# Kernel tuning notes

Measured on AMD Instinct MI355X. Metric: run time of the kernel, lower is better.

The kernel has to match this reference:

```python
import jax, jax.numpy as jnp
import numpy as np

N_HEAD = 16
HEAD_DIM = 64
D_MODEL = N_HEAD * HEAD_DIM  # 1024
B, L = 2, 2048

def setup_inputs() -> dict:
    key = jax.random.key(0)
    k1, k2, k3, k4, k5 = jax.random.split(key, 5)
    s = 0.02
    return {
        "hidden_states": jax.random.normal(k1, (B, L, D_MODEL), dtype=jnp.float32),
        "W_qkv": jax.random.normal(k2, (D_MODEL, 3 * D_MODEL), dtype=jnp.float32) * s,
        "b_qkv": jax.random.normal(k3, (3 * D_MODEL,), dtype=jnp.float32) * s,
        "W_proj": jax.random.normal(k4, (D_MODEL, D_MODEL), dtype=jnp.float32) * s,
        "b_proj": jax.random.normal(k5, (D_MODEL,), dtype=jnp.float32) * s,
        "window_size": 128,
    }

def reference(hidden_states, W_qkv, b_qkv, W_proj, b_proj, window_size):
    Bb, Ll, Dd = hidden_states.shape
    # GPT-2 Conv1D: x @ W + b
    qkv = hidden_states @ W_qkv + b_qkv  # [B, L, 3D]
    q, k, v = jnp.split(qkv, 3, axis=2)
    def to_heads(t):
        return t.reshape(Bb, Ll, N_HEAD, HEAD_DIM).transpose(0, 2, 1, 3)  # [B,H,L,d]
    q, k, v = to_heads(q), to_heads(k), to_heads(v)
    scale = jnp.sqrt(jnp.asarray(HEAD_DIM, dtype=q.dtype))
    scores = jnp.einsum('bhqd,bhkd->bhqk', q, k) / scale  # [B,H,L,L]
    pos = jnp.arange(Ll)
    dist = pos[:, None] - pos[None, :]  # query - key
    sw_mask = (dist < 0) | (dist >= window_size)  # True = masked out
    scores = jnp.where(sw_mask[None, None, :, :], jnp.asarray(-jnp.inf, scores.dtype), scores)
    attn_weights = jax.nn.softmax(scores, axis=-1)  # dropout is identity (eval)
    out = jnp.einsum('bhqk,bhkd->bhqd', attn_weights, v)  # [B,H,L,d]
    out = out.transpose(0, 2, 1, 3).reshape(Bb, Ll, Dd)
    out = out @ W_proj + b_proj
    return (out, attn_weights)
```

## Files before the change

### kernel.cpp

```cpp
#include <hip/hip_runtime.h>
#include <stdint.h>

#define NH 16
#define HD 64
#define DM 1024
#define BB 2
#define LL 2048

typedef __bf16 bf16x8 __attribute__((ext_vector_type(8)));
typedef float f32x4 __attribute__((ext_vector_type(4)));

__device__ __forceinline__ uint16_t f2bf(float f) {
  union { float f; uint32_t u; } x{f};
  uint32_t r = (x.u + 0x7fff + ((x.u >> 16) & 1)) >> 16;
  return (uint16_t)r;
}

__device__ __forceinline__ void gload_lds16(const void* g, void* l) {
  __builtin_amdgcn_global_load_lds(
      (const __attribute__((address_space(1))) unsigned int*)g,
      (__attribute__((address_space(3))) unsigned int*)l, 16, 0, 0);
}

__global__ __launch_bounds__(256) void cvt_bf16(
    const float* __restrict__ x, uint16_t* __restrict__ y, int n4) {
  int i = blockIdx.x * 256 + threadIdx.x;
  if (i >= n4) return;
  float4 v = ((const float4*)x)[i];
  ushort4 o;
  o.x = f2bf(v.x); o.y = f2bf(v.y); o.z = f2bf(v.z); o.w = f2bf(v.w);
  ((ushort4*)y)[i] = o;
}

__global__ __launch_bounds__(256) void transpose_cvt(
    const float* __restrict__ W, uint16_t* __restrict__ WT, int K, int N) {
  __shared__ float t[32][33];
  int bk = blockIdx.y * 32, bn = blockIdx.x * 32;
  int c = threadIdx.x & 31, r0 = threadIdx.x >> 5;
#pragma unroll
  for (int p = 0; p < 4; ++p) {
    int r = r0 + p * 8;
    t[r][c] = W[(size_t)(bk + r) * N + bn + c];
  }
  __syncthreads();
#pragma unroll
  for (int p = 0; p < 4; ++p) {
    int r = r0 + p * 8;
    WT[(size_t)(bn + r) * K + bk + c] = f2bf(t[c][r]);
  }
}

__global__ __launch_bounds__(256) void gemm_bt_bf16(
    const uint16_t* __restrict__ A, const uint16_t* __restrict__ BT,
    const float* __restrict__ bias, float* __restrict__ C,
    int M, int N, int K) {
  __shared__ uint16_t As[128 * 32];
  __shared__ uint16_t Bs[128 * 32];
  const int tid = threadIdx.x;
  const int bm = blockIdx.y * 128, bn = blockIdx.x * 128;
  const int lane = tid & 63, wave = tid >> 6;
  const int wr = wave >> 1, wc = wave & 1;
  f32x4 acc[4][4] = {};

  for (int k0 = 0; k0 < K; k0 += 32) {
#pragma unroll
    for (int c = 0; c < 2; ++c) {
      int e = c * 2048 + tid * 8;
      int r = e >> 5, col = e & 31;
      gload_lds16(A + (size_t)(bm + r) * K + k0 + col, (char*)As + (size_t)e * 2);
      gload_lds16(BT + (size_t)(bn + r) * K + k0 + col, (char*)Bs + (size_t)e * 2);
    }
    __syncthreads();

    const int kseg = (lane >> 4) * 8;
    bf16x8 af[4], bfr[4];
#pragma unroll
    for (int i = 0; i < 4; ++i)
      af[i] = *(const bf16x8*)&As[(wr * 64 + i * 16 + (lane & 15)) * 32 + kseg];
#pragma unroll
    for (int j = 0; j < 4; ++j)
      bfr[j] = *(const bf16x8*)&Bs[(wc * 64 + j * 16 + (lane & 15)) * 32 + kseg];
#pragma unroll
    for (int i = 0; i < 4; ++i)
#pragma unroll
      for (int j = 0; j < 4; ++j)
        acc[i][j] = __builtin_amdgcn_mfma_f32_16x16x32_bf16(af[i], bfr[j], acc[i][j], 0, 0, 0);
    __syncthreads();
  }

#pragma unroll
  for (int i = 0; i < 4; ++i) {
#pragma unroll
    for (int j = 0; j < 4; ++j) {
      int col = bn + wc * 64 + j * 16 + (lane & 15);
      float bv = bias[col];
#pragma unroll
      for (int r = 0; r < 4; ++r) {
        int row = bm + wr * 64 + i * 16 + (lane >> 4) * 4 + r;
        C[(size_t)row * N + col] = acc[i][j][r] + bv;
      }
    }
  }
}

#define QT 32
#define KT 160
#define KS 72
#define PS 168

__global__ __launch_bounds__(256, 4) void attn_sw(
    const float* __restrict__ qkv,
    float* __restrict__ attnw,
    uint16_t* __restrict__ ctxb,
    const int* __restrict__ wsz_p) {
  __shared__ __align__(16) char smemU[KT * KS * 2];
  __shared__ __align__(16) uint16_t Qs[QT * KS];
  __shared__ __align__(16) uint16_t Psb[QT * PS];
  uint16_t* Ksb = (uint16_t*)smemU;
  float* Sf = (float*)smemU;

  const int wsz = *wsz_p;
  const int tid = threadIdx.x;
  const int lane = tid & 63, wave = tid >> 6;
  const int ntile = LL / QT;
  const int qt = blockIdx.x % ntile;
  const int h = (blockIdx.x / ntile) % NH;
  const int b = blockIdx.x / (ntile * NH);
  const int q0 = qt * QT;
  const int kmin = max(0, q0 - (wsz - 1));
  const int kbase = kmin & ~31;

  {
    int r = tid >> 3, c = (tid & 7) * 8;
    const float* src = qkv + (size_t)(b * LL + q0 + r) * (3 * DM) + h * HD + c;
    float4 a = *(const float4*)src, b4 = *(const float4*)(src + 4);
    uint16_t* dst = &Qs[r * KS + c];
    dst[0] = f2bf(a.x); dst[1] = f2bf(a.y); dst[2] = f2bf(a.z); dst[3] = f2bf(a.w);
    dst[4] = f2bf(b4.x); dst[5] = f2bf(b4.y); dst[6] = f2bf(b4.z); dst[7] = f2bf(b4.w);
  }
#pragma unroll
  for (int p = 0; p < 3; ++p) {
    int u = tid + p * 256;
    int r = u >> 2, c = (u & 3) * 16;
    if (r < KT) {
      const float* src = qkv + (size_t)(b * LL + kbase + r) * (3 * DM) + DM + h * HD + c;
      float4 a = *(const float4*)src, b4 = *(const float4*)(src + 4);
      float4 e = *(const float4*)(src + 8), f = *(const float4*)(src + 12);
      uint16_t* dst = &Ksb[r * KS + c];
      dst[0] = f2bf(a.x); dst[1] = f2bf(a.y); dst[2] = f2bf(a.z); dst[3] = f2bf(a.w);
      dst[4] = f2bf(b4.x); dst[5] = f2bf(b4.y); dst[6] = f2bf(b4.z); dst[7] = f2bf(b4.w);
      dst[8] = f2bf(e.x); dst[9] = f2bf(e.y); dst[10] = f2bf(e.z); dst[11] = f2bf(e.w);
      dst[12] = f2bf(f.x); dst[13] = f2bf(f.y); dst[14] = f2bf(f.z); dst[15] = f2bf(f.w);
    }
  }
  __syncthreads();

  const int mt = wave & 1, ntb = (wave >> 1) * 5;
  f32x4 sfrag[5];
  {
    const int kseg = (lane >> 4) * 8;
    bf16x8 aq0 = *(const bf16x8*)&Qs[(mt * 16 + (lane & 15)) * KS + kseg];
    bf16x8 aq1 = *(const bf16x8*)&Qs[(mt * 16 + (lane & 15)) * KS + 32 + kseg];
#pragma unroll
    for (int t = 0; t < 5; ++t) {
      int nt = ntb + t;
      bf16x8 bk0 = *(const bf16x8*)&Ksb[(nt * 16 + (lane & 15)) * KS + kseg];
      bf16x8 bk1 = *(const bf16x8*)&Ksb[(nt * 16 + (lane & 15)) * KS + 32 + kseg];
      f32x4 c = {0.f, 0.f, 0.f, 0.f};
      c = __builtin_amdgcn_mfma_f32_16x16x32_bf16(aq0, bk0, c, 0, 0, 0);
      c = __builtin_amdgcn_mfma_f32_16x16x32_bf16(aq1, bk1, c, 0, 0, 0);
      sfrag[t] = c;
    }
  }
  __syncthreads();

#pragma unroll
  for (int t = 0; t < 5; ++t) {
    int nt = ntb + t;
#pragma unroll
    for (int r = 0; r < 4; ++r)
      Sf[(mt * 16 + (lane >> 4) * 4 + r) * PS + nt * 16 + (lane & 15)] = sfrag[t][r];
  }
  __syncthreads();

  {
    const int qi = tid >> 3;
    const int kg = tid & 7;
    const int q = q0 + qi;
    float s[20];
#pragma unroll
    for (int j = 0; j < 20; ++j) s[j] = Sf[qi * PS + kg + 8 * j];
    float m = -1e30f;
#pragma unroll
    for (int j = 0; j < 20; ++j) {
      int gk = kbase + kg + 8 * j;
      bool valid = (gk <= q) && (gk > q - wsz);
      s[j] = valid ? s[j] * 0.125f : -1e30f;
      m = fmaxf(m, s[j]);
    }
#pragma unroll
    for (int off = 1; off < 8; off <<= 1)
      m = fmaxf(m, __shfl_xor(m, off, 64));
    float l = 0.f;
#pragma unroll
    for (int j = 0; j < 20; ++j) {
      float e = (s[j] > -1e29f) ? __expf(s[j] - m) : 0.f;
      s[j] = e;
      l += e;
    }
#pragma unroll
    for (int off = 1; off < 8; off <<= 1)
      l += __shfl_xor(l, off, 64);
    float inv = 1.f / l;
#pragma unroll
    for (int j = 0; j < 20; ++j) {
      float p = s[j] * inv;
      Sf[qi * PS + kg + 8 * j] = p;
      Psb[qi * PS + kg + 8 * j] = f2bf(p);
    }
  }
  __syncthreads();

  {
#pragma unroll
    for (int it = 0; it < 16; ++it) {
      int r = it * 2 + (tid >> 7);
      size_t rowoff = ((size_t)((b * NH + h) * LL + q0 + r)) * LL;
      int cb = (tid & 127) * 4;
#pragma unroll
      for (int jj = 0; jj < 4; ++jj) {
        int c4 = cb + jj * 512;
        f32x4 v = {0.f, 0.f, 0.f, 0.f};
        int pc = c4 - kbase;
        if (pc >= 0 && pc < KT)
          v = *(const f32x4*)&Sf[r * PS + pc];
        __builtin_nontemporal_store(v, (f32x4*)&attnw[rowoff + c4]);
      }
    }
  }

  {
    const int nt = wave;
    const int kseg = (lane >> 4) * 8;
    f32x4 ofrag[2] = {};
#pragma unroll
    for (int ks = 0; ks < 5; ++ks) {
      const float* vs = qkv + (size_t)(b * LL + kbase + ks * 32 + kseg) * (3 * DM) +
                        2 * DM + h * HD + nt * 16 + (lane & 15);
      uint16_t vb[8];
#pragma unroll
      for (int j = 0; j < 8; ++j) vb[j] = f2bf(vs[(size_t)j * (3 * DM)]);
      bf16x8 bv = *(const bf16x8*)vb;
#pragma unroll
      for (int m = 0; m < 2; ++m) {
        bf16x8 ap = *(const bf16x8*)&Psb[(m * 16 + (lane & 15)) * PS + ks * 32 + kseg];
        ofrag[m] = __builtin_amdgcn_mfma_f32_16x16x32_bf16(ap, bv, ofrag[m], 0, 0, 0);
      }
    }
#pragma unroll
    for (int m = 0; m < 2; ++m)
#pragma unroll
      for (int r = 0; r < 4; ++r) {
        int q = q0 + m * 16 + (lane >> 4) * 4 + r;
        ctxb[(size_t)(b * LL + q) * DM + h * HD + nt * 16 + (lane & 15)] = f2bf(ofrag[m][r]);
      }
  }
}

extern "C" void kernel_launch(void* const* d_in, const int* in_sizes, int n_in,
                              void* d_out, int out_size, void* d_ws, size_t ws_size,
                              hipStream_t stream) {
  const float* hs    = (const float*)d_in[0];
  const float* Wqkv  = (const float*)d_in[1];
  const float* bqkv  = (const float*)d_in[2];
  const float* Wproj = (const float*)d_in[3];
  const float* bproj = (const float*)d_in[4];
  const int*   wszp  = (const int*)d_in[5];

  float* out   = (float*)d_out;
  float* attnw = (float*)d_out + (size_t)BB * LL * DM;

  char* wsb = (char*)d_ws;
  float*    qkv    = (float*)wsb;
  uint16_t* hsctxb = (uint16_t*)(wsb + 50331648);
  uint16_t* WqkvT  = (uint16_t*)(wsb + 50331648 + 8388608);
  uint16_t* WprojT = (uint16_t*)(wsb + 50331648 + 8388608 + 6291456);

  dim3 blk(256);

  cvt_bf16<<<dim3((BB * LL * DM / 4 + 255) / 256), blk, 0, stream>>>(hs, hsctxb, BB * LL * DM / 4);
  transpose_cvt<<<dim3(3 * DM / 32, DM / 32), blk, 0, stream>>>(Wqkv, WqkvT, DM, 3 * DM);
  transpose_cvt<<<dim3(DM / 32, DM / 32), blk, 0, stream>>>(Wproj, WprojT, DM, DM);

  gemm_bt_bf16<<<dim3(3 * DM / 128, BB * LL / 128), blk, 0, stream>>>(
      hsctxb, WqkvT, bqkv, qkv, BB * LL, 3 * DM, DM);

  attn_sw<<<dim3(BB * NH * (LL / QT)), blk, 0, stream>>>(qkv, attnw, hsctxb, wszp);

  gemm_bt_bf16<<<dim3(DM / 128, BB * LL / 128), blk, 0, stream>>>(
      hsctxb, WprojT, bproj, out, BB * LL, DM, DM);
}
```

Baseline: 638.2 us.

## Store QKV as bf16 and split attention-weight expansion into separate kernel

```diff
diff --git a/kernel.cpp b/kernel.cpp
--- a/kernel.cpp
+++ b/kernel.cpp
@@ -14,6 +14,10 @@
   union { float f; uint32_t u; } x{f};
   uint32_t r = (x.u + 0x7fff + ((x.u >> 16) & 1)) >> 16;
   return (uint16_t)r;
+}
+__device__ __forceinline__ float bf2f(uint16_t u) {
+  union { uint32_t u; float f; } x{(uint32_t)u << 16};
+  return x.f;
 }
 
 __device__ __forceinline__ void gload_lds16(const void* g, void* l) {
@@ -52,7 +56,7 @@
 
 __global__ __launch_bounds__(256) void gemm_bt_bf16(
     const uint16_t* __restrict__ A, const uint16_t* __restrict__ BT,
-    const float* __restrict__ bias, float* __restrict__ C,
+    const float* __restrict__ bias, void* __restrict__ Cout, int c_bf16,
     int M, int N, int K) {
   __shared__ uint16_t As[128 * 32];
   __shared__ uint16_t Bs[128 * 32];
@@ -96,8 +100,12 @@
       float bv = bias[col];
 #pragma unroll
       for (int r = 0; r < 4; ++r) {
-        int row = bm + wr * 64 + i * 16 + (lane >> 4) * 4 + r;
-        C[(size_t)row * N + col] = acc[i][j][r] + bv;
+        size_t row = (size_t)(bm + wr * 64 + i * 16 + (lane >> 4) * 4 + r);
+        float v = acc[i][j][r] + bv;
+        if (c_bf16)
+          ((uint16_t*)Cout)[row * N + col] = f2bf(v);
+        else
+          ((float*)Cout)[row * N + col] = v;
       }
     }
   }
@@ -108,9 +116,9 @@
 #define KS 72
 #define PS 168
 
-__global__ __launch_bounds__(256, 4) void attn_sw(
-    const float* __restrict__ qkv,
-    float* __restrict__ attnw,
+__global__ __launch_bounds__(256, 4) void attn_compute(
+    const uint16_t* __restrict__ qkvb,
+    uint16_t* __restrict__ band,
     uint16_t* __restrict__ ctxb,
     const int* __restrict__ wsz_p) {
   __shared__ __align__(16) char smemU[KT * KS * 2];
@@ -127,30 +135,20 @@
   const int h = (blockIdx.x / ntile) % NH;
   const int b = blockIdx.x / (ntile * NH);
   const int q0 = qt * QT;
-  const int kmin = max(0, q0 - (wsz - 1));
-  const int kbase = kmin & ~31;
-
-  {
-    int r = tid >> 3, c = (tid & 7) * 8;
-    const float* src = qkv + (size_t)(b * LL + q0 + r) * (3 * DM) + h * HD + c;
-    float4 a = *(const float4*)src, b4 = *(const float4*)(src + 4);
-    uint16_t* dst = &Qs[r * KS + c];
-    dst[0] = f2bf(a.x); dst[1] = f2bf(a.y); dst[2] = f2bf(a.z); dst[3] = f2bf(a.w);
-    dst[4] = f2bf(b4.x); dst[5] = f2bf(b4.y); dst[6] = f2bf(b4.z); dst[7] = f2bf(b4.w);
-  }
-#pragma unroll
-  for (int p = 0; p < 3; ++p) {
+  const int kbase = max(0, q0 - (wsz - 1)) & ~31;
+
+  if (tid < 256) {
+    int r = tid >> 3, c8 = (tid & 7) * 8;
+    *(bf16x8*)&Qs[r * KS + c8] =
+        *(const bf16x8*)&qkvb[(size_t)(b * LL + q0 + r) * (3 * DM) + h * HD + c8];
+  }
+#pragma unroll
+  for (int p = 0; p < 5; ++p) {
     int u = tid + p * 256;
-    int r = u >> 2, c = (u & 3) * 16;
-    if (r < KT) {
-      const float* src = qkv + (size_t)(b * LL + kbase + r) * (3 * DM) + DM + h * HD + c;
-      float4 a = *(const float4*)src, b4 = *(const float4*)(src + 4);
-      float4 e = *(const float4*)(src + 8), f = *(const float4*)(src + 12);
-      uint16_t* dst = &Ksb[r * KS + c];
-      dst[0] = f2bf(a.x); dst[1] = f2bf(a.y); dst[2] = f2bf(a.z); dst[3] = f2bf(a.w);
-      dst[4] = f2bf(b4.x); dst[5] = f2bf(b4.y); dst[6] = f2bf(b4.z); dst[7] = f2bf(b4.w);
-      dst[8] = f2bf(e.x); dst[9] = f2bf(e.y); dst[10] = f2bf(e.z); dst[11] = f2bf(e.w);
-      dst[12] = f2bf(f.x); dst[13] = f2bf(f.y); dst[14] = f2bf(f.z); dst[15] = f2bf(f.w);
+    if (u < KT * 8) {
+      int r = u >> 3, c8 = (u & 7) * 8;
+      *(bf16x8*)&Ksb[r * KS + c8] =
+          *(const bf16x8*)&qkvb[(size_t)(b * LL + kbase + r) * (3 * DM) + DM + h * HD + c8];
     }
   }
   __syncthreads();
@@ -213,29 +211,18 @@
       l += __shfl_xor(l, off, 64);
     float inv = 1.f / l;
 #pragma unroll
-    for (int j = 0; j < 20; ++j) {
-      float p = s[j] * inv;
-      Sf[qi * PS + kg + 8 * j] = p;
-      Psb[qi * PS + kg + 8 * j] = f2bf(p);
-    }
-  }
-  __syncthreads();
-
-  {
-#pragma unroll
-    for (int it = 0; it < 16; ++it) {
-      int r = it * 2 + (tid >> 7);
-      size_t rowoff = ((size_t)((b * NH + h) * LL + q0 + r)) * LL;
-      int cb = (tid & 127) * 4;
-#pragma unroll
-      for (int jj = 0; jj < 4; ++jj) {
-        int c4 = cb + jj * 512;
-        f32x4 v = {0.f, 0.f, 0.f, 0.f};
-        int pc = c4 - kbase;
-        if (pc >= 0 && pc < KT)
-          v = *(const f32x4*)&Sf[r * PS + pc];
-        __builtin_nontemporal_store(v, (f32x4*)&attnw[rowoff + c4]);
-      }
+    for (int j = 0; j < 20; ++j)
+      Psb[qi * PS + kg + 8 * j] = f2bf(s[j] * inv);
+  }
+  __syncthreads();
+
+#pragma unroll
+  for (int p = 0; p < 3; ++p) {
+    int u = tid + p * 256;
+    if (u < QT * KT / 8) {
+      int r = u / 20, c8 = (u % 20) * 8;
+      *(bf16x8*)(band + (size_t)blockIdx.x * (QT * KT) + (size_t)u * 8) =
+          *(const bf16x8*)&Psb[r * PS + c8];
     }
   }
 
@@ -245,11 +232,11 @@
     f32x4 ofrag[2] = {};
 #pragma unroll
     for (int ks = 0; ks < 5; ++ks) {
-      const float* vs = qkv + (size_t)(b * LL + kbase + ks * 32 + kseg) * (3 * DM) +
-                        2 * DM + h * HD + nt * 16 + (lane & 15);
+      const uint16_t* vs = qkvb + (size_t)(b * LL + kbase + ks * 32 + kseg) * (3 * DM) +
+                           2 * DM + h * HD + nt * 16 + (lane & 15);
       uint16_t vb[8];
 #pragma unroll
-      for (int j = 0; j < 8; ++j) vb[j] = f2bf(vs[(size_t)j * (3 * DM)]);
+      for (int j = 0; j < 8; ++j) vb[j] = vs[(size_t)j * (3 * DM)];
       bf16x8 bv = *(const bf16x8*)vb;
 #pragma unroll
       for (int m = 0; m < 2; ++m) {
@@ -264,6 +251,47 @@
         int q = q0 + m * 16 + (lane >> 4) * 4 + r;
         ctxb[(size_t)(b * LL + q) * DM + h * HD + nt * 16 + (lane & 15)] = f2bf(ofrag[m][r]);
       }
+  }
+}
+
+__global__ __launch_bounds__(256) void expand_attnw(
+    const uint16_t* __restrict__ band, float* __restrict__ attnw,
+    const int* __restrict__ wsz_p) {
+  __shared__ __align__(16) uint16_t Pb[QT * KT];
+  const int wsz = *wsz_p;
+  const int tid = threadIdx.x;
+  const int ntile = LL / QT;
+  const int qt = blockIdx.x % ntile;
+  const int h = (blockIdx.x / ntile) % NH;
+  const int b = blockIdx.x / (ntile * NH);
+  const int q0 = qt * QT;
+  const int kbase = max(0, q0 - (wsz - 1)) & ~31;
+
+#pragma unroll
+  for (int p = 0; p < 3; ++p) {
+    int u = tid + p * 256;
+    if (u < QT * KT / 8)
+      *(bf16x8*)&Pb[u * 8] =
+          *(const bf16x8*)(band + (size_t)blockIdx.x * (QT * KT) + (size_t)u * 8);
+  }
+  __syncthreads();
+
+#pragma unroll
+  for (int it = 0; it < 16; ++it) {
+    int r = it * 2 + (tid >> 7);
+    size_t rowoff = ((size_t)((b * NH + h) * LL + q0 + r)) * LL;
+    int cb = (tid & 127) * 4;
+#pragma unroll
+    for (int jj = 0; jj < 4; ++jj) {
+      int c4 = cb + jj * 512;
+      f32x4 v = {0.f, 0.f, 0.f, 0.f};
+      int pc = c4 - kbase;
+      if (pc >= 0 && pc < KT) {
+        ushort4 t = *(const ushort4*)&Pb[r * KT + pc];
+        v[0] = bf2f(t.x); v[1] = bf2f(t.y); v[2] = bf2f(t.z); v[3] = bf2f(t.w);
+      }
+      __builtin_nontemporal_store(v, (f32x4*)&attnw[rowoff + c4]);
+    }
   }
 }
 
@@ -281,10 +309,11 @@
   float* attnw = (float*)d_out + (size_t)BB * LL * DM;
 
   char* wsb = (char*)d_ws;
-  float*    qkv    = (float*)wsb;
-  uint16_t* hsctxb = (uint16_t*)(wsb + 50331648);
-  uint16_t* WqkvT  = (uint16_t*)(wsb + 50331648 + 8388608);
-  uint16_t* WprojT = (uint16_t*)(wsb + 50331648 + 8388608 + 6291456);
+  uint16_t* qkvb   = (uint16_t*)wsb;
+  uint16_t* hsctxb = (uint16_t*)(wsb + 25165824);
+  uint16_t* WqkvT  = (uint16_t*)(wsb + 25165824 + 8388608);
+  uint16_t* WprojT = (uint16_t*)(wsb + 25165824 + 8388608 + 6291456);
+  uint16_t* band   = (uint16_t*)(wsb + 25165824 + 8388608 + 6291456 + 2097152);
 
   dim3 blk(256);
 
@@ -293,10 +322,12 @@
   transpose_cvt<<<dim3(DM / 32, DM / 32), blk, 0, stream>>>(Wproj, WprojT, DM, DM);
 
   gemm_bt_bf16<<<dim3(3 * DM / 128, BB * LL / 128), blk, 0, stream>>>(
-      hsctxb, WqkvT, bqkv, qkv, BB * LL, 3 * DM, DM);
-
-  attn_sw<<<dim3(BB * NH * (LL / QT)), blk, 0, stream>>>(qkv, attnw, hsctxb, wszp);
+      hsctxb, WqkvT, bqkv, qkvb, 1, BB * LL, 3 * DM, DM);
+
+  attn_compute<<<dim3(BB * NH * (LL / QT)), blk, 0, stream>>>(qkvb, band, hsctxb, wszp);
 
   gemm_bt_bf16<<<dim3(DM / 128, BB * LL / 128), blk, 0, stream>>>(
-      hsctxb, WprojT, bproj, out, BB * LL, DM, DM);
-}
+      hsctxb, WprojT, bproj, out, 0, BB * LL, DM, DM);
+
+  expand_attnw<<<dim3(BB * NH * (LL / QT)), blk, 0, stream>>>(band, attnw, wszp);
+}
```

Measured after the change: 658.9 us. 1.03x slower.
